# Optimization experiments

Measured on AMD Instinct MI355X. Metric: run time of the kernel, lower is better.

The kernel has to match this reference:

```python
import jax, jax.numpy as jnp
import numpy as np

PAD = 1
STRIDE = 1


def setup_inputs() -> dict:
    key = jax.random.key(0)
    kx, kw, kb = jax.random.split(key, 3)
    C_IN, C_OUT, K, H, W = 128, 256, 3, 256, 256
    lim = 1.0 / np.sqrt(C_IN * K * K)
    x = jax.random.normal(kx, (C_IN, H, W), dtype=jnp.float32)
    weight = jax.random.uniform(kw, (C_OUT, C_IN, K, K), minval=-lim, maxval=lim, dtype=jnp.float32)
    bias = jax.random.uniform(kb, (C_OUT, 1, 1), minval=-lim, maxval=lim, dtype=jnp.float32)
    return {"x": x, "weight": weight, "bias": bias}


def reference(x, weight, bias):
    # Original does per-channel jnp.pad then a scan-based im2col + einsum
    # 'oijk,ihwjk->ohw'. That is exactly a standard cross-correlation conv,
    # expressed here with the efficient fused primitive (same math).
    out = jax.lax.conv_general_dilated(
        x[None],                      # (1, c, h, w)
        weight,                       # (o, i, k, k)
        window_strides=(STRIDE, STRIDE),
        padding=[(PAD, PAD), (PAD, PAD)],
        dimension_numbers=("NCHW", "OIHW", "NCHW"),
    )[0]                              # (o, h', w')
    return out + bias
```

## Files before the change

### kernel.cpp

```cpp
#include <hip/hip_runtime.h>
#include <hip/hip_bf16.h>
#include <stdint.h>


#define CIN   128
#define COUT  256
#define HH    256
#define WW    256
#define HP    258
#define WP    258
#define XP_ELEMS (HP * WP * CIN)

typedef __attribute__((ext_vector_type(8))) __bf16 bf16x8;
typedef __attribute__((ext_vector_type(4))) float  floatx4;
typedef __attribute__((ext_vector_type(8))) short  short8;

#define AS1 __attribute__((address_space(1)))
#define AS3 __attribute__((address_space(3)))

__global__ __launch_bounds__(256) void prep(const float* __restrict__ x,
                                            const float* __restrict__ w,
                                            unsigned short* __restrict__ xp,
                                            unsigned short* __restrict__ wpk) {
    __shared__ __align__(16) unsigned short tile[64][136];
    const int bid = blockIdx.x;
    const int t   = threadIdx.x;
    if (bid < 1024) {
        int h  = bid >> 2;
        int w0 = (bid & 3) << 6;
        int wl = t & 63, icq = t >> 6;
        const float* src = x + h * WW + w0 + wl;
#pragma unroll
        for (int icb = 0; icb < 32; ++icb) {
            int ic = icb * 4 + icq;
            __hip_bfloat16 b = __float2bfloat16(src[ic * (HH * WW)]);
            tile[wl][ic] = __builtin_bit_cast(unsigned short, b);
        }
        __syncthreads();
        int wl2 = t >> 2, q = t & 3;
        const short8* s8 = (const short8*)&tile[wl2][q * 32];
        short8* d8 = (short8*)(xp + ((size_t)(h + 1) * WP + (w0 + 1) + wl2) * CIN + q * 32);
#pragma unroll
        for (int i = 0; i < 4; ++i) d8[i] = s8[i];
    } else if (bid < 2176) {
        int idx = (bid - 1024) * 256 + t;
        int kk  = idx >> 15;
        int rem = idx & 32767;
        __hip_bfloat16 b = __float2bfloat16(w[rem * 9 + kk]);
        wpk[idx] = __builtin_bit_cast(unsigned short, b);
    } else {
        int cid = (bid - 2176) * 256 + t;
        if (cid < 16448) {
            int p = cid >> 4, oct = cid & 15;
            int hp, wp;
            if (p < 258)      { hp = 0;   wp = p; }
            else if (p < 516) { hp = 257; wp = p - 258; }
            else { int s = p - 516; hp = 1 + (s >> 1); wp = (s & 1) * 257; }
            short8 z = {0, 0, 0, 0, 0, 0, 0, 0};
            *(short8*)(xp + ((size_t)hp * WP + wp) * CIN + oct * 8) = z;
        }
    }
}

__global__ __launch_bounds__(512, 2) void conv_mfma(
    const unsigned short* __restrict__ xp,
    const unsigned short* __restrict__ wpk,
    const float* __restrict__ bias,
    float* __restrict__ out) {
    __shared__ __align__(16) unsigned short x_lds[2 * 32768];

    const int tid  = threadIdx.x;
    const int lane = tid & 63;
    const int wv   = tid >> 6;
    const int l15  = lane & 15;
    const int lg   = lane >> 4;
    const int wave_m = (wv >> 2) << 7;
    const int wave_n = (wv & 3) << 6;

    const int orig = blockIdx.x;
    const int h    = ((orig & 7) << 5) | (orig >> 3);

    const int soff = (tid >> 3) * CIN + ((((tid & 7) ^ ((tid >> 3) & 7))) << 3);

    auto stage = [&](int buf, int kk, int kh, int kw, int hf) {
        unsigned short* base = x_lds + buf * 32768;
        const unsigned short* asrc = wpk + (size_t)kk * (COUT * CIN) + hf * 64 + soff;
        const unsigned short* bsrc = xp + ((size_t)(h + kh) * WP + kw) * CIN + hf * 64 + soff;
#pragma unroll
        for (int i = 0; i < 4; ++i)
            __builtin_amdgcn_global_load_lds(
                (const AS1 void*)(asrc + i * 8192),
                (AS3 void*)(base + i * 4096 + tid * 8), 16, 0, 0);
#pragma unroll
        for (int i = 0; i < 4; ++i)
            __builtin_amdgcn_global_load_lds(
                (const AS1 void*)(bsrc + i * 8192),
                (AS3 void*)(base + 16384 + i * 4096 + tid * 8), 16, 0, 0);
    };

    floatx4 acc[8][4];
#pragma unroll
    for (int fi = 0; fi < 8; ++fi)
#pragma unroll
        for (int fj = 0; fj < 4; ++fj) {
            floatx4 z = {0.f, 0.f, 0.f, 0.f};
            acc[fi][fj] = z;
        }

    const int aoct = (lg ^ (l15 & 7)) << 3;

    stage(0, 0, 0, 0, 0);
    __syncthreads();

#pragma unroll
    for (int t2 = 0; t2 < 18; ++t2) {
        const int cur = t2 & 1;

        if (t2 < 17) {
            const int tn  = t2 + 1;
            const int kkn = tn >> 1, hfn = tn & 1;
            const int khn = kkn / 3, kwn = kkn - khn * 3;
            stage(cur ^ 1, kkn, khn, kwn, hfn);
        }

        const unsigned short* Ab = x_lds + cur * 32768;
#pragma unroll
        for (int ks = 0; ks < 2; ++ks) {
            const int kx = ks << 5;
            bf16x8 a[8], b[4];
#pragma unroll
            for (int fj = 0; fj < 4; ++fj)
                b[fj] = *(const bf16x8*)(
                    Ab + 16384 + ((wave_n + fj * 16 + l15) << 6) + (aoct ^ kx));
#pragma unroll
            for (int fi = 0; fi < 8; ++fi)
                a[fi] = *(const bf16x8*)(
                    Ab + ((wave_m + fi * 16 + l15) << 6) + (aoct ^ kx));

            __builtin_amdgcn_s_setprio(1);
#pragma unroll
            for (int fi = 0; fi < 8; ++fi)
#pragma unroll
                for (int fj = 0; fj < 4; ++fj)
                    acc[fi][fj] = __builtin_amdgcn_mfma_f32_16x16x32_bf16(
                        a[fi], b[fj], acc[fi][fj], 0, 0, 0);
            __builtin_amdgcn_s_setprio(0);
        }

        __syncthreads();
    }

    const int nbase = h * WW + wave_n + l15;
#pragma unroll
    for (int fi = 0; fi < 8; ++fi) {
        int mrow = wave_m + fi * 16 + lg * 4;
#pragma unroll
        for (int r = 0; r < 4; ++r) {
            float bv = bias[mrow + r];
#pragma unroll
            for (int fj = 0; fj < 4; ++fj)
                out[(size_t)(mrow + r) * (HH * WW) + nbase + fj * 16] = acc[fi][fj][r] + bv;
        }
    }
}

extern "C" void kernel_launch(void* const* d_in, const int* in_sizes, int n_in,
                              void* d_out, int out_size, void* d_ws, size_t ws_size,
                              hipStream_t stream) {
    (void)in_sizes; (void)n_in; (void)out_size; (void)ws_size;
    const float* x    = (const float*)d_in[0];
    const float* w    = (const float*)d_in[1];
    const float* bias = (const float*)d_in[2];
    float* out = (float*)d_out;

    unsigned short* xp  = (unsigned short*)d_ws;
    unsigned short* wpk = xp + XP_ELEMS;

    prep<<<dim3(2241), dim3(256), 0, stream>>>(x, w, xp, wpk);
    conv_mfma<<<dim3(256), dim3(512), 0, stream>>>(xp, wpk, bias, out);
}
```

Baseline: 131.9 us.

## Interleave LDS prefetch loads with MFMA sub-phases using fine-grained barriers

Splits each K-step of the conv GEMM into four sub-phases. Each sub-phase issues a slice of the next stage's global-to-LDS loads, then runs a quarter of the MFMA work, with explicit s_waitcnt vmcnt counts and raw s_barrier calls in place of __syncthreads. The aim is to spread memory traffic across the compute instead of issuing every load up front, and to cut register pressure by holding only four A fragments at a time. The cost is more barriers per iteration and reliance on hand-counted vmcnt ordering, which is fragile if the compiler reorders loads.

```diff
diff --git a/kernel.cpp b/kernel.cpp
--- a/kernel.cpp
+++ b/kernel.cpp
@@ -81,22 +81,14 @@
     const int h    = ((orig & 7) << 5) | (orig >> 3);
 
     const int soff = (tid >> 3) * CIN + ((((tid & 7) ^ ((tid >> 3) & 7))) << 3);
-
-    auto stage = [&](int buf, int kk, int kh, int kw, int hf) {
-        unsigned short* base = x_lds + buf * 32768;
-        const unsigned short* asrc = wpk + (size_t)kk * (COUT * CIN) + hf * 64 + soff;
-        const unsigned short* bsrc = xp + ((size_t)(h + kh) * WP + kw) * CIN + hf * 64 + soff;
-#pragma unroll
-        for (int i = 0; i < 4; ++i)
-            __builtin_amdgcn_global_load_lds(
-                (const AS1 void*)(asrc + i * 8192),
-                (AS3 void*)(base + i * 4096 + tid * 8), 16, 0, 0);
-#pragma unroll
-        for (int i = 0; i < 4; ++i)
-            __builtin_amdgcn_global_load_lds(
-                (const AS1 void*)(bsrc + i * 8192),
-                (AS3 void*)(base + 16384 + i * 4096 + tid * 8), 16, 0, 0);
-    };
+    const int aoct = (lg ^ (l15 & 7)) << 3;
+
+#define GLD_A(nb_, src_, i_) \
+    __builtin_amdgcn_global_load_lds((const AS1 void*)((src_) + (i_) * 8192), \
+        (AS3 void*)((nb_) + (i_) * 4096 + tid * 8), 16, 0, 0)
+#define GLD_B(nb_, src_, i_) \
+    __builtin_amdgcn_global_load_lds((const AS1 void*)((src_) + (i_) * 8192), \
+        (AS3 void*)((nb_) + 16384 + (i_) * 4096 + tid * 8), 16, 0, 0)
 
     floatx4 acc[8][4];
 #pragma unroll
@@ -107,48 +99,98 @@
             acc[fi][fj] = z;
         }
 
-    const int aoct = (lg ^ (l15 & 7)) << 3;
-
-    stage(0, 0, 0, 0, 0);
-    __syncthreads();
+    {
+        const unsigned short* a0 = wpk + soff;
+        const unsigned short* b0s = xp + ((size_t)h * WP) * CIN + soff;
+        unsigned short* nb = x_lds;
+        GLD_A(nb, a0, 0); GLD_A(nb, a0, 2);
+        GLD_B(nb, b0s, 0); GLD_B(nb, b0s, 1); GLD_B(nb, b0s, 2); GLD_B(nb, b0s, 3);
+        GLD_A(nb, a0, 1); GLD_A(nb, a0, 3);
+    }
+    asm volatile("s_waitcnt vmcnt(2)" ::: "memory");
+    __builtin_amdgcn_s_barrier();
 
 #pragma unroll
     for (int t2 = 0; t2 < 18; ++t2) {
         const int cur = t2 & 1;
-
-        if (t2 < 17) {
-            const int tn  = t2 + 1;
-            const int kkn = tn >> 1, hfn = tn & 1;
-            const int khn = kkn / 3, kwn = kkn - khn * 3;
-            stage(cur ^ 1, kkn, khn, kwn, hfn);
-        }
-
         const unsigned short* Ab = x_lds + cur * 32768;
-#pragma unroll
-        for (int ks = 0; ks < 2; ++ks) {
-            const int kx = ks << 5;
-            bf16x8 a[8], b[4];
-#pragma unroll
-            for (int fj = 0; fj < 4; ++fj)
-                b[fj] = *(const bf16x8*)(
-                    Ab + 16384 + ((wave_n + fj * 16 + l15) << 6) + (aoct ^ kx));
-#pragma unroll
-            for (int fi = 0; fi < 8; ++fi)
-                a[fi] = *(const bf16x8*)(
-                    Ab + ((wave_m + fi * 16 + l15) << 6) + (aoct ^ kx));
-
-            __builtin_amdgcn_s_setprio(1);
-#pragma unroll
-            for (int fi = 0; fi < 8; ++fi)
-#pragma unroll
-                for (int fj = 0; fj < 4; ++fj)
-                    acc[fi][fj] = __builtin_amdgcn_mfma_f32_16x16x32_bf16(
-                        a[fi], b[fj], acc[fi][fj], 0, 0, 0);
-            __builtin_amdgcn_s_setprio(0);
-        }
-
-        __syncthreads();
-    }
+        unsigned short* nb = x_lds + (cur ^ 1) * 32768;
+        const bool hn = (t2 < 17);
+        const int tn  = t2 + 1;
+        const int kkn = tn >> 1, hfn = tn & 1;
+        const int khn = kkn / 3, kwn = kkn - khn * 3;
+        const unsigned short* asrcn = wpk + (size_t)kkn * (COUT * CIN) + hfn * 64 + soff;
+        const unsigned short* bsrcn = xp + ((size_t)(h + khn) * WP + kwn) * CIN + hfn * 64 + soff;
+
+        bf16x8 b0[4], b1[4], a[4];
+
+#pragma unroll
+        for (int fj = 0; fj < 4; ++fj)
+            b0[fj] = *(const bf16x8*)(Ab + 16384 + ((wave_n + fj * 16 + l15) << 6) + aoct);
+#pragma unroll
+        for (int i = 0; i < 4; ++i)
+            a[i] = *(const bf16x8*)(Ab + ((wave_m + i * 16 + l15) << 6) + aoct);
+        if (hn) { GLD_A(nb, asrcn, 0); GLD_A(nb, asrcn, 2); }
+        __builtin_amdgcn_s_barrier();
+        __builtin_amdgcn_s_setprio(1);
+#pragma unroll
+        for (int i = 0; i < 4; ++i)
+#pragma unroll
+            for (int fj = 0; fj < 4; ++fj)
+                acc[i][fj] = __builtin_amdgcn_mfma_f32_16x16x32_bf16(a[i], b0[fj], acc[i][fj], 0, 0, 0);
+        __builtin_amdgcn_s_setprio(0);
+        if (hn) asm volatile("s_waitcnt vmcnt(2)" ::: "memory");
+        else    asm volatile("s_waitcnt vmcnt(0)" ::: "memory");
+        __builtin_amdgcn_s_barrier();
+
+#pragma unroll
+        for (int i = 0; i < 4; ++i)
+            a[i] = *(const bf16x8*)(Ab + ((wave_m + 64 + i * 16 + l15) << 6) + aoct);
+        if (hn) { GLD_B(nb, bsrcn, 0); GLD_B(nb, bsrcn, 1); }
+        __builtin_amdgcn_s_barrier();
+        __builtin_amdgcn_s_setprio(1);
+#pragma unroll
+        for (int i = 0; i < 4; ++i)
+#pragma unroll
+            for (int fj = 0; fj < 4; ++fj)
+                acc[4 + i][fj] = __builtin_amdgcn_mfma_f32_16x16x32_bf16(a[i], b0[fj], acc[4 + i][fj], 0, 0, 0);
+        __builtin_amdgcn_s_setprio(0);
+        __builtin_amdgcn_s_barrier();
+
+#pragma unroll
+        for (int fj = 0; fj < 4; ++fj)
+            b1[fj] = *(const bf16x8*)(Ab + 16384 + ((wave_n + fj * 16 + l15) << 6) + (aoct ^ 32));
+#pragma unroll
+        for (int i = 0; i < 4; ++i)
+            a[i] = *(const bf16x8*)(Ab + ((wave_m + i * 16 + l15) << 6) + (aoct ^ 32));
+        if (hn) { GLD_B(nb, bsrcn, 2); GLD_B(nb, bsrcn, 3); }
+        __builtin_amdgcn_s_barrier();
+        __builtin_amdgcn_s_setprio(1);
+#pragma unroll
+        for (int i = 0; i < 4; ++i)
+#pragma unroll
+            for (int fj = 0; fj < 4; ++fj)
+                acc[i][fj] = __builtin_amdgcn_mfma_f32_16x16x32_bf16(a[i], b1[fj], acc[i][fj], 0, 0, 0);
+        __builtin_amdgcn_s_setprio(0);
+        __builtin_amdgcn_s_barrier();
+
+#pragma unroll
+        for (int i = 0; i < 4; ++i)
+            a[i] = *(const bf16x8*)(Ab + ((wave_m + 64 + i * 16 + l15) << 6) + (aoct ^ 32));
+        if (hn) { GLD_A(nb, asrcn, 1); GLD_A(nb, asrcn, 3); }
+        __builtin_amdgcn_s_barrier();
+        __builtin_amdgcn_s_setprio(1);
+#pragma unroll
+        for (int i = 0; i < 4; ++i)
+#pragma unroll
+            for (int fj = 0; fj < 4; ++fj)
+                acc[4 + i][fj] = __builtin_amdgcn_mfma_f32_16x16x32_bf16(a[i], b1[fj], acc[4 + i][fj], 0, 0, 0);
+        __builtin_amdgcn_s_setprio(0);
+        if (hn) asm volatile("s_waitcnt vmcnt(2)" ::: "memory");
+        __builtin_amdgcn_s_barrier();
+    }
+#undef GLD_A
+#undef GLD_B
 
     const int nbase = h * WW + wave_n + l15;
 #pragma unroll
```

Result: faster. 129.3 us (-2.0%).

## Use 4 waves per block with 128x128 per-wave tiles and early LDS fragment loads

Applied to the files above, without the earlier changes.

Cuts the conv block from 8 waves to 4, so each wave now computes a 128x128 output tile (8x8 MFMA fragments) instead of 128x64, which doubles register reuse of the A/B fragments. The k=0 fragments are read from LDS before the next stage's global-to-LDS prefetch is issued, and both k-halves are loaded before the MFMA burst. The cost is 256 accumulator floats per lane, which forces one block per CU and lowers latency hiding. It may also cause register spills.

```diff
diff --git a/kernel.cpp b/kernel.cpp
--- a/kernel.cpp
+++ b/kernel.cpp
@@ -62,7 +62,7 @@
     }
 }
 
-__global__ __launch_bounds__(512, 2) void conv_mfma(
+__global__ __launch_bounds__(256, 1) void conv_mfma(
     const unsigned short* __restrict__ xp,
     const unsigned short* __restrict__ wpk,
     const float* __restrict__ bias,
@@ -74,40 +74,41 @@
     const int wv   = tid >> 6;
     const int l15  = lane & 15;
     const int lg   = lane >> 4;
-    const int wave_m = (wv >> 2) << 7;
-    const int wave_n = (wv & 3) << 6;
+    const int wave_m = (wv >> 1) << 7;
+    const int wave_n = (wv & 1) << 7;
 
     const int orig = blockIdx.x;
     const int h    = ((orig & 7) << 5) | (orig >> 3);
 
     const int soff = (tid >> 3) * CIN + ((((tid & 7) ^ ((tid >> 3) & 7))) << 3);
+    const int aoct = (lg ^ (l15 & 7)) << 3;
+
+#define GLD(dst_, src_) \
+    __builtin_amdgcn_global_load_lds((const AS1 void*)(src_), \
+        (AS3 void*)((dst_) + tid * 8), 16, 0, 0)
+#define LDA(Ab_, mb_, kx_) \
+    (*(const bf16x8*)((Ab_) + (((mb_) + l15) << 6) + (aoct ^ (kx_))))
+#define LDB(Ab_, nb2_, kx_) \
+    (*(const bf16x8*)((Ab_) + 16384 + (((nb2_) + l15) << 6) + (aoct ^ (kx_))))
 
     auto stage = [&](int buf, int kk, int kh, int kw, int hf) {
-        unsigned short* base = x_lds + buf * 32768;
+        unsigned short* nb = x_lds + buf * 32768;
         const unsigned short* asrc = wpk + (size_t)kk * (COUT * CIN) + hf * 64 + soff;
         const unsigned short* bsrc = xp + ((size_t)(h + kh) * WP + kw) * CIN + hf * 64 + soff;
 #pragma unroll
-        for (int i = 0; i < 4; ++i)
-            __builtin_amdgcn_global_load_lds(
-                (const AS1 void*)(asrc + i * 8192),
-                (AS3 void*)(base + i * 4096 + tid * 8), 16, 0, 0);
+        for (int i = 0; i < 8; ++i) GLD(nb + i * 2048, asrc + i * 32 * CIN);
 #pragma unroll
-        for (int i = 0; i < 4; ++i)
-            __builtin_amdgcn_global_load_lds(
-                (const AS1 void*)(bsrc + i * 8192),
-                (AS3 void*)(base + 16384 + i * 4096 + tid * 8), 16, 0, 0);
+        for (int i = 0; i < 8; ++i) GLD(nb + 16384 + i * 2048, bsrc + i * 32 * CIN);
     };
 
-    floatx4 acc[8][4];
+    floatx4 acc[8][8];
 #pragma unroll
     for (int fi = 0; fi < 8; ++fi)
 #pragma unroll
-        for (int fj = 0; fj < 4; ++fj) {
+        for (int fj = 0; fj < 8; ++fj) {
             floatx4 z = {0.f, 0.f, 0.f, 0.f};
             acc[fi][fj] = z;
         }
-
-    const int aoct = (lg ^ (l15 & 7)) << 3;
 
     stage(0, 0, 0, 0, 0);
     __syncthreads();
@@ -115,6 +116,13 @@
 #pragma unroll
     for (int t2 = 0; t2 < 18; ++t2) {
         const int cur = t2 & 1;
+        const unsigned short* Ab = x_lds + cur * 32768;
+
+        bf16x8 a0[8], b0[8], a1[8], b1[8];
+#pragma unroll
+        for (int fj = 0; fj < 8; ++fj) b0[fj] = LDB(Ab, wave_n + fj * 16, 0);
+#pragma unroll
+        for (int fi = 0; fi < 8; ++fi) a0[fi] = LDA(Ab, wave_m + fi * 16, 0);
 
         if (t2 < 17) {
             const int tn  = t2 + 1;
@@ -123,32 +131,31 @@
             stage(cur ^ 1, kkn, khn, kwn, hfn);
         }
 
-        const unsigned short* Ab = x_lds + cur * 32768;
 #pragma unroll
-        for (int ks = 0; ks < 2; ++ks) {
-            const int kx = ks << 5;
-            bf16x8 a[8], b[4];
+        for (int fj = 0; fj < 8; ++fj) b1[fj] = LDB(Ab, wave_n + fj * 16, 32);
 #pragma unroll
-            for (int fj = 0; fj < 4; ++fj)
-                b[fj] = *(const bf16x8*)(
-                    Ab + 16384 + ((wave_n + fj * 16 + l15) << 6) + (aoct ^ kx));
+        for (int fi = 0; fi < 8; ++fi) a1[fi] = LDA(Ab, wave_m + fi * 16, 32);
+
+        __builtin_amdgcn_s_setprio(1);
 #pragma unroll
-            for (int fi = 0; fi < 8; ++fi)
-                a[fi] = *(const bf16x8*)(
-                    Ab + ((wave_m + fi * 16 + l15) << 6) + (aoct ^ kx));
-
-            __builtin_amdgcn_s_setprio(1);
+        for (int fi = 0; fi < 8; ++fi)
 #pragma unroll
-            for (int fi = 0; fi < 8; ++fi)
+            for (int fj = 0; fj < 8; ++fj)
+                acc[fi][fj] = __builtin_amdgcn_mfma_f32_16x16x32_bf16(
+                    a0[fi], b0[fj], acc[fi][fj], 0, 0, 0);
 #pragma unroll
-                for (int fj = 0; fj < 4; ++fj)
-                    acc[fi][fj] = __builtin_amdgcn_mfma_f32_16x16x32_bf16(
-                        a[fi], b[fj], acc[fi][fj], 0, 0, 0);
-            __builtin_amdgcn_s_setprio(0);
-        }
+        for (int fi = 0; fi < 8; ++fi)
+#pragma unroll
+            for (int fj = 0; fj < 8; ++fj)
+                acc[fi][fj] = __builtin_amdgcn_mfma_f32_16x16x32_bf16(
+                    a1[fi], b1[fj], acc[fi][fj], 0, 0, 0);
+        __builtin_amdgcn_s_setprio(0);
 
         __syncthreads();
     }
+#undef GLD
+#undef LDA
+#undef LDB
 
     const int nbase = h * WW + wave_n + l15;
 #pragma unroll
@@ -158,7 +165,7 @@
         for (int r = 0; r < 4; ++r) {
             float bv = bias[mrow + r];
 #pragma unroll
-            for (int fj = 0; fj < 4; ++fj)
+            for (int fj = 0; fj < 8; ++fj)
                 out[(size_t)(mrow + r) * (HH * WW) + nbase + fj * 16] = acc[fi][fj][r] + bv;
         }
     }
@@ -177,5 +184,5 @@
     unsigned short* wpk = xp + XP_ELEMS;
 
     prep<<<dim3(2241), dim3(256), 0, stream>>>(x, w, xp, wpk);
-    conv_mfma<<<dim3(256), dim3(512), 0, stream>>>(xp, wpk, bias, out);
+    conv_mfma<<<dim3(256), dim3(256), 0, stream>>>(xp, wpk, bias, out);
 }
```

Measured after the change: 131.6 us. Within noise of the previous version (-0.2%).
